# Optimization experiments

Hardware: AMD Instinct MI355X
Metric: run time of the kernel (lower is better)

The kernel has to match this reference:

```python
import jax, jax.numpy as jnp
import numpy as np

N_TOK = 2048      # flattened batch*seq tokens
D_MODEL = 1024    # in_features
D_INT = 512       # d_intermediate
N_EXPERTS = 8     # n_routed_experts
TOP_K = 2         # n_activated_experts


def setup_inputs() -> dict:
    key = jax.random.key(0)
    k1, k2, k3, k4, k5 = jax.random.split(key, 5)
    x = jax.random.normal(k1, (N_TOK, D_MODEL), dtype=jnp.float32)
    indices = jax.random.randint(k2, (N_TOK, TOP_K), 0, N_EXPERTS, dtype=jnp.int32)
    # router combine weights (normalized over top-k like a softmax router)
    weights = jax.nn.softmax(jax.random.normal(k3, (N_TOK, TOP_K), dtype=jnp.float32), axis=-1)
    # tokens-per-expert counts, consistent with indices (as the router would supply)
    counts = jnp.bincount(indices.reshape(-1), length=N_EXPERTS).astype(jnp.int32)
    # expert weights: fc1 -> 2*d_int (gated MLP), fc2 -> d_model; kaiming-ish scale
    s1 = 1.0 / np.sqrt(D_MODEL)
    s2 = 1.0 / np.sqrt(D_INT)
    fc1_weight = jax.random.uniform(k4, (N_EXPERTS, 2 * D_INT, D_MODEL), jnp.float32, -s1, s1)
    fc2_weight = jax.random.uniform(k5, (N_EXPERTS, D_MODEL, D_INT), jnp.float32, -s2, s2)
    return {"x": x, "weights": weights, "indices": indices, "counts": counts,
            "fc1_weight": fc1_weight, "fc2_weight": fc2_weight}


def reference(x, weights, indices, counts, fc1_weight, fc2_weight):
    # Dense dispatch-free formulation: run every token through every expert's
    # gated MLP, then gather the per-slot expert output. Identical math to the
    # sort / grouped-GEMM / scatter path for the selected (token, expert) pairs.
    # h: (n_tok, n_experts, 2*d_int)
    h = jnp.einsum('td,egd->teg', x, fc1_weight)
    y, z = jnp.split(h, 2, axis=-1)
    a = y * jax.nn.silu(z)  # GatedMLP: y * activation(z)
    # expert outputs: (n_tok, n_experts, d_model)
    out = jnp.einsum('tei,edi->ted', a, fc2_weight)
    # gather the chosen expert output for each of the top-k slots: (n_tok, k, d_model)
    per_slot = jnp.take_along_axis(out, indices[:, :, None], axis=1)
    # combine: z = bmm(weights[:, None], x_by_expert).squeeze(1)
    return jnp.einsum('tk,tkd->td', weights, per_slot)
```

## Files before the change

### kernel.cpp

```cpp
#include <hip/hip_runtime.h>

typedef unsigned short u16;
typedef unsigned int u32;
using short8  = __attribute__((ext_vector_type(8))) short;
using floatx4 = __attribute__((ext_vector_type(4))) float;

#define N_TOK   2048
#define D_MODEL 1024
#define D_INT   512
#define NE      8
#define ROWS_PAD 5120

#define O_META   0
#define O_ROWOF  4096
#define O_PAIR   20480
#define O_XG     65536
#define O_ACT    10551296
#define O_FC1B   36765696
#define O_FC2B   53542912

static __device__ inline u16 f2bf(float f) {
    u32 u = __builtin_bit_cast(u32, f);
    u = (u + 0x7fffu + ((u >> 16) & 1u)) >> 16;
    return (u16)u;
}
static __device__ inline u32 pack2(float a, float b) {
    return (u32)f2bf(a) | ((u32)f2bf(b) << 16);
}
static __device__ inline void glds16(const u16* g, u16* l) {
    __builtin_amdgcn_global_load_lds(
        (const __attribute__((address_space(1))) void*)g,
        (__attribute__((address_space(3))) void*)l, 16, 0, 0);
}

__global__ __launch_bounds__(256) void route_kernel(const int* __restrict__ indices,
                                                    const int* __restrict__ counts,
                                                    int* __restrict__ meta,
                                                    int* __restrict__ row_of,
                                                    int* __restrict__ pair_of) {
    __shared__ int cnt[256][NE];
    __shared__ int off[NE];
    int t = threadIdx.x;
    #pragma unroll
    for (int i = 0; i < 20; i++) pair_of[t * 20 + i] = -1;
    int idx[16];
    #pragma unroll
    for (int i = 0; i < 16; i++) idx[i] = indices[t * 16 + i];
    int loc[NE];
    #pragma unroll
    for (int e = 0; e < NE; e++) {
        int c = 0;
        #pragma unroll
        for (int i = 0; i < 16; i++) c += (idx[i] == e);
        loc[e] = c;
        cnt[t][e] = c;
    }
    if (t == 0) {
        int acc = 0;
        #pragma unroll
        for (int e = 0; e < NE; e++) {
            off[e] = acc;
            meta[e] = acc;
            acc += ((counts[e] + 127) >> 7) << 7;
        }
        meta[8] = acc;
    }
    __syncthreads();
    for (int d = 1; d < 256; d <<= 1) {
        int v[NE];
        #pragma unroll
        for (int e = 0; e < NE; e++) v[e] = (t >= d) ? cnt[t - d][e] : 0;
        __syncthreads();
        #pragma unroll
        for (int e = 0; e < NE; e++) cnt[t][e] += v[e];
        __syncthreads();
    }
    #pragma unroll
    for (int e = 0; e < NE; e++) cnt[t][e] -= loc[e];
    __syncthreads();
    #pragma unroll
    for (int i = 0; i < 16; i++) {
        int e = idx[i];
        int r = cnt[t][e]++;
        int row = off[e] + r;
        row_of[t * 16 + i] = row;
        pair_of[row] = t * 16 + i;
    }
}

__global__ __launch_bounds__(128) void gather_kernel(const float* __restrict__ x,
                                                     const int* __restrict__ row_of,
                                                     u16* __restrict__ Xg) {
    int t = blockIdx.x;
    int tid = threadIdx.x;
    int r0 = row_of[2 * t], r1 = row_of[2 * t + 1];
    const floatx4* src = reinterpret_cast<const floatx4*>(x + (size_t)t * D_MODEL);
    floatx4 a = src[tid * 2];
    floatx4 b = src[tid * 2 + 1];
    uint4 o;
    o.x = pack2(a[0], a[1]); o.y = pack2(a[2], a[3]);
    o.z = pack2(b[0], b[1]); o.w = pack2(b[2], b[3]);
    *reinterpret_cast<uint4*>(Xg + (size_t)r0 * D_MODEL + tid * 8) = o;
    *reinterpret_cast<uint4*>(Xg + (size_t)r1 * D_MODEL + tid * 8) = o;
}

__global__ void convert_w(const float* __restrict__ fc1, const float* __restrict__ fc2,
                          u16* __restrict__ fc1b, u16* __restrict__ fc2b) {
    size_t v = (size_t)blockIdx.x * 256 + threadIdx.x;
    const float* src; u16* dst; size_t off;
    if (v < 1048576) { src = fc1; dst = fc1b; off = v * 8; }
    else             { src = fc2; dst = fc2b; off = (v - 1048576) * 8; }
    const floatx4* s4 = reinterpret_cast<const floatx4*>(src + off);
    floatx4 a = s4[0], b = s4[1];
    uint4 o;
    o.x = pack2(a[0], a[1]); o.y = pack2(a[2], a[3]);
    o.z = pack2(b[0], b[1]); o.w = pack2(b[2], b[3]);
    *reinterpret_cast<uint4*>(dst + off) = o;
}

__global__ __launch_bounds__(256) void gemm1_kernel(
    const u16* __restrict__ Xg, const u16* __restrict__ fc1b,
    u16* __restrict__ Act, const int* __restrict__ meta) {
    __shared__ u16 As[4096];
    __shared__ u16 Bs[4096];
    __shared__ int soff[9];
    int tid = threadIdx.x;
    if (tid < 9) soff[tid] = meta[tid];
    __syncthreads();
    int row0 = blockIdx.y * 128;
    if (row0 >= soff[8]) return;
    int e = 0;
    while (soff[e + 1] <= row0) e++;
    int bx = blockIdx.x;
    const u16* A  = Xg + (size_t)row0 * 1024;
    const u16* Be = fc1b + (size_t)e * 1024 * 1024;

    int lane = tid & 63, w = tid >> 6;
    int m0 = (w >> 1) * 64, n0 = (w & 1) * 32;
    int lr = lane & 15, kq = lane >> 4;
    int ka = ((kq ^ ((lr >> 1) & 3)) * 8);

    int v0 = tid, v1 = tid + 256;
    int r0s = v0 >> 2, kb0 = (v0 & 3) ^ ((r0s >> 1) & 3);
    int r1s = v1 >> 2, kb1 = (v1 & 3) ^ ((r1s >> 1) & 3);
    int brow0 = (r0s < 64) ? bx * 64 + r0s : 448 + bx * 64 + r0s;
    int brow1 = (r1s < 64) ? bx * 64 + r1s : 448 + bx * 64 + r1s;
    u16* lA0 = As + (w * 64) * 8;
    u16* lA1 = As + (w * 64 + 256) * 8;
    u16* lB0 = Bs + (w * 64) * 8;
    u16* lB1 = Bs + (w * 64 + 256) * 8;
    const u16* gA0 = A + (size_t)r0s * 1024 + kb0 * 8;
    const u16* gA1 = A + (size_t)r1s * 1024 + kb1 * 8;
    const u16* gB0 = Be + (size_t)brow0 * 1024 + kb0 * 8;
    const u16* gB1 = Be + (size_t)brow1 * 1024 + kb1 * 8;

    floatx4 acc[4][4];
    #pragma unroll
    for (int i = 0; i < 4; i++)
        #pragma unroll
        for (int j = 0; j < 4; j++) acc[i][j] = (floatx4){0.f, 0.f, 0.f, 0.f};

    for (int k0 = 0; k0 < 1024; k0 += 32) {
        glds16(gA0 + k0, lA0);
        glds16(gA1 + k0, lA1);
        glds16(gB0 + k0, lB0);
        glds16(gB1 + k0, lB1);
        __syncthreads();
        short8 af[4], bf[4];
        #pragma unroll
        for (int i = 0; i < 4; i++)
            af[i] = *reinterpret_cast<const short8*>(&As[(m0 + i * 16 + lr) * 32 + ka]);
        #pragma unroll
        for (int j = 0; j < 4; j++) {
            int nn = (j < 2) ? (n0 + j * 16) : (64 + n0 + (j - 2) * 16);
            bf[j] = *reinterpret_cast<const short8*>(&Bs[(nn + lr) * 32 + ka]);
        }
        #pragma unroll
        for (int i = 0; i < 4; i++)
            #pragma unroll
            for (int j = 0; j < 4; j++)
                acc[i][j] = __builtin_amdgcn_mfma_f32_16x16x32_bf16(af[i], bf[j], acc[i][j], 0, 0, 0);
        __syncthreads();
    }
    #pragma unroll
    for (int i = 0; i < 4; i++) {
        #pragma unroll
        for (int jy = 0; jy < 2; jy++) {
            floatx4 y = acc[i][jy], z = acc[i][jy + 2];
            #pragma unroll
            for (int r = 0; r < 4; r++) {
                float zz = z[r];
                float av = y[r] * (zz / (1.0f + __expf(-zz)));
                int m = m0 + i * 16 + kq * 4 + r;
                int g = bx * 64 + n0 + jy * 16 + lr;
                Act[(size_t)(row0 + m) * D_INT + g] = f2bf(av);
            }
        }
    }
}

__global__ __launch_bounds__(256) void gemm2_kernel(
    const u16* __restrict__ Act, const u16* __restrict__ fc2b,
    float* __restrict__ out, const int* __restrict__ meta,
    const int* __restrict__ pair_of, const float* __restrict__ wts) {
    __shared__ u16 As[4096];
    __shared__ u16 Bs[4096];
    __shared__ int soff[9];
    __shared__ int sPair[128];
    __shared__ float sW[128];
    int tid = threadIdx.x;
    if (tid < 9) soff[tid] = meta[tid];
    __syncthreads();
    int row0 = blockIdx.y * 128;
    if (row0 >= soff[8]) return;
    int e = 0;
    while (soff[e + 1] <= row0) e++;
    int bx = blockIdx.x;
    const u16* A  = Act + (size_t)row0 * 512;
    const u16* Be = fc2b + (size_t)e * 1024 * 512;

    int lane = tid & 63, w = tid >> 6;
    int m0 = (w >> 1) * 64, n0 = (w & 1) * 64;
    int lr = lane & 15, kq = lane >> 4;
    int ka = ((kq ^ ((lr >> 1) & 3)) * 8);

    int v0 = tid, v1 = tid + 256;
    int r0s = v0 >> 2, kb0 = (v0 & 3) ^ ((r0s >> 1) & 3);
    int r1s = v1 >> 2, kb1 = (v1 & 3) ^ ((r1s >> 1) & 3);
    u16* lA0 = As + (w * 64) * 8;
    u16* lA1 = As + (w * 64 + 256) * 8;
    u16* lB0 = Bs + (w * 64) * 8;
    u16* lB1 = Bs + (w * 64 + 256) * 8;
    const u16* gA0 = A + (size_t)r0s * 512 + kb0 * 8;
    const u16* gA1 = A + (size_t)r1s * 512 + kb1 * 8;
    const u16* gB0 = Be + (size_t)(bx * 128 + r0s) * 512 + kb0 * 8;
    const u16* gB1 = Be + (size_t)(bx * 128 + r1s) * 512 + kb1 * 8;

    floatx4 acc[4][4];
    #pragma unroll
    for (int i = 0; i < 4; i++)
        #pragma unroll
        for (int j = 0; j < 4; j++) acc[i][j] = (floatx4){0.f, 0.f, 0.f, 0.f};

    for (int k0 = 0; k0 < 512; k0 += 32) {
        glds16(gA0 + k0, lA0);
        glds16(gA1 + k0, lA1);
        glds16(gB0 + k0, lB0);
        glds16(gB1 + k0, lB1);
        __syncthreads();
        short8 af[4], bf[4];
        #pragma unroll
        for (int i = 0; i < 4; i++)
            af[i] = *reinterpret_cast<const short8*>(&As[(m0 + i * 16 + lr) * 32 + ka]);
        #pragma unroll
        for (int j = 0; j < 4; j++)
            bf[j] = *reinterpret_cast<const short8*>(&Bs[(n0 + j * 16 + lr) * 32 + ka]);
        #pragma unroll
        for (int i = 0; i < 4; i++)
            #pragma unroll
            for (int j = 0; j < 4; j++)
                acc[i][j] = __builtin_amdgcn_mfma_f32_16x16x32_bf16(af[i], bf[j], acc[i][j], 0, 0, 0);
        __syncthreads();
    }
    if (tid < 128) {
        int p = pair_of[row0 + tid];
        sPair[tid] = p;
        sW[tid] = (p >= 0) ? wts[p] : 0.f;
    }
    __syncthreads();
    #pragma unroll
    for (int i = 0; i < 4; i++)
        #pragma unroll
        for (int r = 0; r < 4; r++) {
            int m = m0 + i * 16 + kq * 4 + r;
            int p = sPair[m];
            if (p >= 0) {
                float wgt = sW[m];
                float* dst = out + (size_t)(p >> 1) * D_MODEL + bx * 128;
                #pragma unroll
                for (int j = 0; j < 4; j++)
                    atomicAdd(dst + n0 + j * 16 + lr, wgt * acc[i][j][r]);
            }
        }
}

extern "C" void kernel_launch(void* const* d_in, const int* in_sizes, int n_in,
                              void* d_out, int out_size, void* d_ws, size_t ws_size,
                              hipStream_t stream) {
    const float* x       = (const float*)d_in[0];
    const float* wts     = (const float*)d_in[1];
    const int*   indices = (const int*)d_in[2];
    const int*   counts  = (const int*)d_in[3];
    const float* fc1     = (const float*)d_in[4];
    const float* fc2     = (const float*)d_in[5];
    float* out = (float*)d_out;
    char* ws = (char*)d_ws;

    int*  meta    = (int*)(ws + O_META);
    int*  row_of  = (int*)(ws + O_ROWOF);
    int*  pair_of = (int*)(ws + O_PAIR);
    u16*  Xg      = (u16*)(ws + O_XG);
    u16*  Act     = (u16*)(ws + O_ACT);
    u16*  fc1b    = (u16*)(ws + O_FC1B);
    u16*  fc2b    = (u16*)(ws + O_FC2B);

    hipMemsetAsync(d_out, 0, (size_t)out_size * sizeof(float), stream);
    route_kernel<<<1, 256, 0, stream>>>(indices, counts, meta, row_of, pair_of);
    convert_w<<<6144, 256, 0, stream>>>(fc1, fc2, fc1b, fc2b);
    gather_kernel<<<N_TOK, 128, 0, stream>>>(x, row_of, Xg);
    gemm1_kernel<<<dim3(8, 40), 256, 0, stream>>>(Xg, fc1b, Act, meta);
    gemm2_kernel<<<dim3(8, 40), 256, 0, stream>>>(Act, fc2b, out, meta, pair_of, wts);
}
```

Baseline: 163.6 us.

## Fuse routing, gather, weight conversion and output zeroing into one prep kernel

Replaces the memset, the single-block routing scan, the weight-conversion kernel and the gather kernel with one prep kernel whose block ranges do weight conversion, per-token slot computation plus gather, and output zeroing. Each token block finds its row within its expert by counting earlier matching indices over the whole index array, which removes the serial one-block scan and its dependency chain. The GEMM kernels now derive expert offsets from counts directly and use per-row token and weight arrays instead of pair_of. This trades fewer launches and serialization for redundant per-token index scans.

```diff
diff --git a/kernel.cpp b/kernel.cpp
--- a/kernel.cpp
+++ b/kernel.cpp
@@ -11,9 +11,8 @@
 #define NE      8
 #define ROWS_PAD 5120
 
-#define O_META   0
-#define O_ROWOF  4096
-#define O_PAIR   20480
+#define O_TOK    0
+#define O_WROW   24576
 #define O_XG     65536
 #define O_ACT    10551296
 #define O_FC1B   36765696
@@ -33,102 +32,91 @@
         (__attribute__((address_space(3))) void*)l, 16, 0, 0);
 }
 
-__global__ __launch_bounds__(256) void route_kernel(const int* __restrict__ indices,
-                                                    const int* __restrict__ counts,
-                                                    int* __restrict__ meta,
-                                                    int* __restrict__ row_of,
-                                                    int* __restrict__ pair_of) {
-    __shared__ int cnt[256][NE];
-    __shared__ int off[NE];
-    int t = threadIdx.x;
-    #pragma unroll
-    for (int i = 0; i < 20; i++) pair_of[t * 20 + i] = -1;
-    int idx[16];
-    #pragma unroll
-    for (int i = 0; i < 16; i++) idx[i] = indices[t * 16 + i];
-    int loc[NE];
-    #pragma unroll
-    for (int e = 0; e < NE; e++) {
-        int c = 0;
-        #pragma unroll
-        for (int i = 0; i < 16; i++) c += (idx[i] == e);
-        loc[e] = c;
-        cnt[t][e] = c;
-    }
-    if (t == 0) {
-        int acc = 0;
-        #pragma unroll
-        for (int e = 0; e < NE; e++) {
-            off[e] = acc;
-            meta[e] = acc;
-            acc += ((counts[e] + 127) >> 7) << 7;
-        }
-        meta[8] = acc;
-    }
-    __syncthreads();
-    for (int d = 1; d < 256; d <<= 1) {
-        int v[NE];
-        #pragma unroll
-        for (int e = 0; e < NE; e++) v[e] = (t >= d) ? cnt[t - d][e] : 0;
-        __syncthreads();
-        #pragma unroll
-        for (int e = 0; e < NE; e++) cnt[t][e] += v[e];
-        __syncthreads();
-    }
-    #pragma unroll
-    for (int e = 0; e < NE; e++) cnt[t][e] -= loc[e];
-    __syncthreads();
-    #pragma unroll
-    for (int i = 0; i < 16; i++) {
-        int e = idx[i];
-        int r = cnt[t][e]++;
-        int row = off[e] + r;
-        row_of[t * 16 + i] = row;
-        pair_of[row] = t * 16 + i;
-    }
-}
-
-__global__ __launch_bounds__(128) void gather_kernel(const float* __restrict__ x,
-                                                     const int* __restrict__ row_of,
-                                                     u16* __restrict__ Xg) {
-    int t = blockIdx.x;
-    int tid = threadIdx.x;
-    int r0 = row_of[2 * t], r1 = row_of[2 * t + 1];
-    const floatx4* src = reinterpret_cast<const floatx4*>(x + (size_t)t * D_MODEL);
-    floatx4 a = src[tid * 2];
-    floatx4 b = src[tid * 2 + 1];
-    uint4 o;
-    o.x = pack2(a[0], a[1]); o.y = pack2(a[2], a[3]);
-    o.z = pack2(b[0], b[1]); o.w = pack2(b[2], b[3]);
-    *reinterpret_cast<uint4*>(Xg + (size_t)r0 * D_MODEL + tid * 8) = o;
-    *reinterpret_cast<uint4*>(Xg + (size_t)r1 * D_MODEL + tid * 8) = o;
-}
-
-__global__ void convert_w(const float* __restrict__ fc1, const float* __restrict__ fc2,
-                          u16* __restrict__ fc1b, u16* __restrict__ fc2b) {
-    size_t v = (size_t)blockIdx.x * 256 + threadIdx.x;
-    const float* src; u16* dst; size_t off;
-    if (v < 1048576) { src = fc1; dst = fc1b; off = v * 8; }
-    else             { src = fc2; dst = fc2b; off = (v - 1048576) * 8; }
-    const floatx4* s4 = reinterpret_cast<const floatx4*>(src + off);
-    floatx4 a = s4[0], b = s4[1];
-    uint4 o;
-    o.x = pack2(a[0], a[1]); o.y = pack2(a[2], a[3]);
-    o.z = pack2(b[0], b[1]); o.w = pack2(b[2], b[3]);
-    *reinterpret_cast<uint4*>(dst + off) = o;
+__global__ __launch_bounds__(256) void prep_kernel(
+    const float* __restrict__ x, const float* __restrict__ wts,
+    const int* __restrict__ indices, const int* __restrict__ counts,
+    const float* __restrict__ fc1, const float* __restrict__ fc2,
+    u16* __restrict__ fc1b, u16* __restrict__ fc2b,
+    u16* __restrict__ Xg, int* __restrict__ tok, float* __restrict__ wrow,
+    float* __restrict__ out) {
+    int b = blockIdx.x, tid = threadIdx.x;
+    if (b < 6144) {
+        size_t v = (size_t)b * 256 + tid;
+        const float* src; u16* dst; size_t off;
+        if (v < 1048576) { src = fc1; dst = fc1b; off = v * 8; }
+        else             { src = fc2; dst = fc2b; off = (v - 1048576) * 8; }
+        const floatx4* s4 = reinterpret_cast<const floatx4*>(src + off);
+        floatx4 a = s4[0], bb = s4[1];
+        uint4 o;
+        o.x = pack2(a[0], a[1]); o.y = pack2(a[2], a[3]);
+        o.z = pack2(bb[0], bb[1]); o.w = pack2(bb[2], bb[3]);
+        *reinterpret_cast<uint4*>(dst + off) = o;
+        return;
+    }
+    if (b < 8192) {
+        int t = b - 6144;
+        int off[NE];
+        {
+            int acc = 0;
+            #pragma unroll
+            for (int e = 0; e < NE; e++) { off[e] = acc; acc += ((counts[e] + 127) >> 7) << 7; }
+        }
+        int e0 = indices[2 * t], e1 = indices[2 * t + 1];
+        __shared__ int s0, s1;
+        if (tid == 0) { s0 = 0; s1 = 0; }
+        __syncthreads();
+        int c0 = 0, c1 = 0;
+        const int4* ip = reinterpret_cast<const int4*>(indices);
+        #pragma unroll
+        for (int i = 0; i < 4; i++) {
+            int4 vv = ip[tid * 4 + i];
+            int q = tid * 16 + i * 4;
+            c0 += (q + 0 < 2 * t && vv.x == e0) + (q + 1 < 2 * t && vv.y == e0)
+                + (q + 2 < 2 * t && vv.z == e0) + (q + 3 < 2 * t && vv.w == e0);
+            c1 += (q + 0 <= 2 * t && vv.x == e1) + (q + 1 <= 2 * t && vv.y == e1)
+                + (q + 2 <= 2 * t && vv.z == e1) + (q + 3 <= 2 * t && vv.w == e1);
+        }
+        if (c0) atomicAdd(&s0, c0);
+        if (c1) atomicAdd(&s1, c1);
+        __syncthreads();
+        int r0 = off[e0] + s0;
+        int r1 = off[e1] + s1;
+        if (tid == 0) {
+            tok[r0] = t; tok[r1] = t;
+            wrow[r0] = wts[2 * t]; wrow[r1] = wts[2 * t + 1];
+        }
+        const floatx4* src = reinterpret_cast<const floatx4*>(x + (size_t)t * D_MODEL);
+        floatx4 a = src[tid];
+        uint2 o;
+        o.x = pack2(a[0], a[1]); o.y = pack2(a[2], a[3]);
+        *reinterpret_cast<uint2*>(Xg + (size_t)r0 * D_MODEL + tid * 4) = o;
+        *reinterpret_cast<uint2*>(Xg + (size_t)r1 * D_MODEL + tid * 4) = o;
+        return;
+    }
+    {
+        int z = b - 8192;
+        floatx4* dst = reinterpret_cast<floatx4*>(out) + (size_t)z * 1024;
+        #pragma unroll
+        for (int i = 0; i < 4; i++) dst[i * 256 + tid] = (floatx4){0.f, 0.f, 0.f, 0.f};
+        return;
+    }
 }
 
 __global__ __launch_bounds__(256) void gemm1_kernel(
     const u16* __restrict__ Xg, const u16* __restrict__ fc1b,
-    u16* __restrict__ Act, const int* __restrict__ meta) {
+    u16* __restrict__ Act, const int* __restrict__ counts) {
     __shared__ u16 As[4096];
     __shared__ u16 Bs[4096];
-    __shared__ int soff[9];
     int tid = threadIdx.x;
-    if (tid < 9) soff[tid] = meta[tid];
-    __syncthreads();
+    int soff[NE + 1];
+    {
+        int acc = 0;
+        #pragma unroll
+        for (int e2 = 0; e2 < NE; e2++) { soff[e2] = acc; acc += ((counts[e2] + 127) >> 7) << 7; }
+        soff[NE] = acc;
+    }
     int row0 = blockIdx.y * 128;
-    if (row0 >= soff[8]) return;
+    if (row0 >= soff[NE]) return;
     int e = 0;
     while (soff[e + 1] <= row0) e++;
     int bx = blockIdx.x;
@@ -201,18 +189,26 @@
 
 __global__ __launch_bounds__(256) void gemm2_kernel(
     const u16* __restrict__ Act, const u16* __restrict__ fc2b,
-    float* __restrict__ out, const int* __restrict__ meta,
-    const int* __restrict__ pair_of, const float* __restrict__ wts) {
+    float* __restrict__ out, const int* __restrict__ counts,
+    const int* __restrict__ tok, const float* __restrict__ wrow) {
     __shared__ u16 As[4096];
     __shared__ u16 Bs[4096];
-    __shared__ int soff[9];
-    __shared__ int sPair[128];
+    __shared__ int sTok[128];
     __shared__ float sW[128];
     int tid = threadIdx.x;
-    if (tid < 9) soff[tid] = meta[tid];
-    __syncthreads();
+    int soff[NE + 1];
+    int cnt[NE];
+    {
+        int acc = 0;
+        #pragma unroll
+        for (int e2 = 0; e2 < NE; e2++) {
+            soff[e2] = acc; cnt[e2] = counts[e2];
+            acc += ((cnt[e2] + 127) >> 7) << 7;
+        }
+        soff[NE] = acc;
+    }
     int row0 = blockIdx.y * 128;
-    if (row0 >= soff[8]) return;
+    if (row0 >= soff[NE]) return;
     int e = 0;
     while (soff[e + 1] <= row0) e++;
     int bx = blockIdx.x;
@@ -263,9 +259,10 @@
         __syncthreads();
     }
     if (tid < 128) {
-        int p = pair_of[row0 + tid];
-        sPair[tid] = p;
-        sW[tid] = (p >= 0) ? wts[p] : 0.f;
+        int g = row0 + tid;
+        bool val = (g - soff[e]) < cnt[e];
+        sTok[tid] = val ? tok[g] : -1;
+        sW[tid]   = val ? wrow[g] : 0.f;
     }
     __syncthreads();
     #pragma unroll
@@ -273,10 +270,10 @@
         #pragma unroll
         for (int r = 0; r < 4; r++) {
             int m = m0 + i * 16 + kq * 4 + r;
-            int p = sPair[m];
-            if (p >= 0) {
+            int t = sTok[m];
+            if (t >= 0) {
                 float wgt = sW[m];
-                float* dst = out + (size_t)(p >> 1) * D_MODEL + bx * 128;
+                float* dst = out + (size_t)t * D_MODEL + bx * 128;
                 #pragma unroll
                 for (int j = 0; j < 4; j++)
                     atomicAdd(dst + n0 + j * 16 + lr, wgt * acc[i][j][r]);
@@ -296,18 +293,15 @@
     float* out = (float*)d_out;
     char* ws = (char*)d_ws;
 
-    int*  meta    = (int*)(ws + O_META);
-    int*  row_of  = (int*)(ws + O_ROWOF);
-    int*  pair_of = (int*)(ws + O_PAIR);
-    u16*  Xg      = (u16*)(ws + O_XG);
-    u16*  Act     = (u16*)(ws + O_ACT);
-    u16*  fc1b    = (u16*)(ws + O_FC1B);
-    u16*  fc2b    = (u16*)(ws + O_FC2B);
-
-    hipMemsetAsync(d_out, 0, (size_t)out_size * sizeof(float), stream);
-    route_kernel<<<1, 256, 0, stream>>>(indices, counts, meta, row_of, pair_of);
-    convert_w<<<6144, 256, 0, stream>>>(fc1, fc2, fc1b, fc2b);
-    gather_kernel<<<N_TOK, 128, 0, stream>>>(x, row_of, Xg);
-    gemm1_kernel<<<dim3(8, 40), 256, 0, stream>>>(Xg, fc1b, Act, meta);
-    gemm2_kernel<<<dim3(8, 40), 256, 0, stream>>>(Act, fc2b, out, meta, pair_of, wts);
-}
+    int*   tok  = (int*)(ws + O_TOK);
+    float* wrow = (float*)(ws + O_WROW);
+    u16*   Xg   = (u16*)(ws + O_XG);
+    u16*   Act  = (u16*)(ws + O_ACT);
+    u16*   fc1b = (u16*)(ws + O_FC1B);
+    u16*   fc2b = (u16*)(ws + O_FC2B);
+
+    prep_kernel<<<8704, 256, 0, stream>>>(x, wts, indices, counts, fc1, fc2,
+                                          fc1b, fc2b, Xg, tok, wrow, out);
+    gemm1_kernel<<<dim3(8, 40), 256, 0, stream>>>(Xg, fc1b, Act, counts);
+    gemm2_kernel<<<dim3(8, 40), 256, 0, stream>>>(Act, fc2b, out, counts, tok, wrow);
+}
```

Measured after the change: 159.1 us. 1.03x faster.
